# Optimization experiments

Hardware: AMD Instinct MI355X
Metric: run time of the kernel (lower is better)

Reference implementation:

```python
import jax, jax.numpy as jnp
import numpy as np

B, D, K = 8, 128, 7          # batch, num objects, per-object feature
Q = 256                      # question embedding size
G0, G1 = 511, 512            # g-layer sizes
F1, F2, OUT = 512, 1024, 16  # f-layer sizes


def setup_inputs() -> dict:
    key = jax.random.key(0)
    ks = jax.random.split(key, 14)
    def lin(kw, kb, fan_in, fan_out):
        lim = 1.0 / np.sqrt(fan_in)
        w = jax.random.uniform(kw, (fan_in, fan_out), jnp.float32, -lim, lim)
        b = jax.random.uniform(kb, (fan_out,), jnp.float32, -lim, lim)
        return w, b
    x = jax.random.normal(ks[0], (B, D, K), jnp.float32)
    qst = jax.random.normal(ks[1], (B, Q), jnp.float32)
    g0_w, g0_b = lin(ks[2], ks[3], 2 * K, G0)
    g1_w, g1_b = lin(ks[4], ks[5], G0 + Q, G1)
    f1_w, f1_b = lin(ks[6], ks[7], G1, F1)
    f2_w, f2_b = lin(ks[8], ks[9], F1, F2)
    f3_w, f3_b = lin(ks[10], ks[11], F2, OUT)
    return {"x": x, "qst": qst,
            "g0_w": g0_w, "g0_b": g0_b, "g1_w": g1_w, "g1_b": g1_b,
            "f1_w": f1_w, "f1_b": f1_b, "f2_w": f2_w, "f2_b": f2_b,
            "f3_w": f3_w, "f3_b": f3_b}


def reference(x, qst, g0_w, g0_b, g1_w, g1_b, f1_w, f1_b, f2_w, f2_b, f3_w, f3_b):
    b, d, k = x.shape
    # all-pairs: torch x_i[b,a,c,:]=x[b,c,:], x_j[b,a,c,:]=x[b,a,:]
    x_i = jnp.broadcast_to(x[:, None, :, :], (b, d, d, k))
    x_j = jnp.broadcast_to(x[:, :, None, :], (b, d, d, k))
    pairs = jnp.concatenate([x_i, x_j], axis=-1)            # (b,d,d,2k)
    h = jax.nn.relu(pairs @ g0_w + g0_b)                    # (b,d,d,G0)
    q = jnp.broadcast_to(qst[:, None, None, :], (b, d, d, qst.shape[-1]))
    h = jnp.concatenate([h, q], axis=-1)                    # (b,d,d,G0+Q)
    h = jax.nn.relu(h @ g1_w + g1_b)                        # (b,d,d,G1)
    x_g = h.sum(axis=(1, 2))                                # sum over d^2 pairs -> (b,G1)
    f = jax.nn.relu(x_g @ f1_w + f1_b)
    f = jax.nn.relu(f @ f2_w + f2_b)                        # dropout = identity (eval)
    logits = f @ f3_w + f3_b
    return jax.nn.log_softmax(logits, axis=1)
```

## Files before the change

kernel.cpp:

```cpp
#include <hip/hip_runtime.h>
#include <hip/hip_bf16.h>

#define B_  8
#define D_  128
#define K_  7
#define Q_  256
#define G0_ 511
#define G0P 512
#define G1_ 512
#define F1_ 512
#define F2_ 1024
#define OUT_ 16

typedef __bf16 bf16x8 __attribute__((ext_vector_type(8)));
typedef float  f32x4  __attribute__((ext_vector_type(4)));

#define GL2LDS(g, l) __builtin_amdgcn_global_load_lds(                        \
    (const __attribute__((address_space(1))) void*)(g),                       \
    (__attribute__((address_space(3))) void*)(l), 16, 0, 0)

__global__ void k_prep(const float* __restrict__ x, const float* __restrict__ g0w,
                       const float* __restrict__ g0b, const float* __restrict__ qst,
                       const float* __restrict__ g1w, const float* __restrict__ g1b,
                       const float* __restrict__ f1w, const float* __restrict__ f2w,
                       const float* __restrict__ f3w,
                       float* __restrict__ u, float* __restrict__ v,
                       __bf16* __restrict__ w1t, float* __restrict__ qterm,
                       float* __restrict__ xg, float* __restrict__ f1t,
                       float* __restrict__ f2t, float* __restrict__ f3t) {
    const int blk = blockIdx.x;
    const int t   = threadIdx.x;
    if (blk < 1024) {
        __shared__ float xs[8];
        if (t < K_) xs[t] = x[blk * K_ + t];
        __syncthreads();
        #pragma unroll
        for (int h = 0; h < 2; ++h) {
            const int g = t + h * 256;
            float su = 0.f, sv = 0.f;
            if (g < G0_) {
                #pragma unroll
                for (int k = 0; k < K_; ++k) {
                    su += xs[k] * g0w[k * G0_ + g];
                    sv += xs[k] * g0w[(K_ + k) * G0_ + g];
                }
                su += g0b[g];
            }
            u[blk * G0P + g] = (g < G0_) ? su : 0.f;
            v[blk * G0P + g] = (g < G0_) ? sv : 0.f;
        }
    } else if (blk < 1280) {
        __shared__ __bf16 tile[32][33];
        const int bb = blk - 1024;
        const int bx = bb & 15, by = bb >> 4;
        const int r = t >> 5, c = t & 31;
        #pragma unroll
        for (int i = 0; i < 4; ++i) {
            const int k = by * 32 + r + i * 8;
            const int n = bx * 32 + c;
            tile[r + i * 8][c] = (__bf16)((k < G0_) ? g1w[k * G1_ + n] : 0.f);
        }
        __syncthreads();
        #pragma unroll
        for (int i = 0; i < 4; ++i) {
            const int n = bx * 32 + r + i * 8;
            const int cc = (c >> 3) & 3, j = c & 7;
            const int slot = cc ^ ((n >> 1) & 3);
            w1t[by * 16384 + n * 32 + slot * 8 + j] = tile[c][r + i * 8];
        }
    } else if (blk < 1312) {
        __shared__ float qs[256];
        __shared__ float red[2][128];
        const int qb = blk - 1280;
        const int b = qb >> 2, nb = (qb & 3) << 7;
        qs[t] = qst[b * Q_ + t];
        __syncthreads();
        const int n = nb + (t & 127);
        const int qh = (t >> 7) * 128;
        float s = 0.f;
        #pragma unroll 8
        for (int q = 0; q < 128; ++q)
            s += qs[qh + q] * g1w[(G0_ + qh + q) * G1_ + n];
        red[t >> 7][t & 127] = s;
        __syncthreads();
        if (t < 128)
            qterm[b * G1_ + nb + t] = red[0][t] + red[1][t] + g1b[nb + t];
    } else if (blk < 1320) {
        const int b = blk - 1312;
        xg[b * G1_ + t] = 0.f;
        xg[b * G1_ + 256 + t] = 0.f;
    } else if (blk < 1576) {
        __shared__ float tile[32][33];
        const int j = blk - 1320;
        const int bo = j & 15, bk = j >> 4;
        const int r = t >> 5, c = t & 31;
        #pragma unroll
        for (int i = 0; i < 4; ++i)
            tile[r + i * 8][c] = f1w[(bk * 32 + r + i * 8) * F1_ + bo * 32 + c];
        __syncthreads();
        #pragma unroll
        for (int i = 0; i < 4; ++i)
            f1t[(bo * 32 + r + i * 8) * G1_ + bk * 32 + c] = tile[c][r + i * 8];
    } else if (blk < 2088) {
        __shared__ float tile[32][33];
        const int j = blk - 1576;
        const int bo = j & 31, bk = j >> 5;
        const int r = t >> 5, c = t & 31;
        #pragma unroll
        for (int i = 0; i < 4; ++i)
            tile[r + i * 8][c] = f2w[(bk * 32 + r + i * 8) * F2_ + bo * 32 + c];
        __syncthreads();
        #pragma unroll
        for (int i = 0; i < 4; ++i)
            f2t[(bo * 32 + r + i * 8) * F1_ + bk * 32 + c] = tile[c][r + i * 8];
    } else {
        const int k = (blk - 2088) * 256 + t;
        float4 r0 = *(const float4*)(f3w + k * OUT_);
        float4 r1 = *(const float4*)(f3w + k * OUT_ + 4);
        float4 r2 = *(const float4*)(f3w + k * OUT_ + 8);
        float4 r3 = *(const float4*)(f3w + k * OUT_ + 12);
        const float rr[16] = {r0.x,r0.y,r0.z,r0.w, r1.x,r1.y,r1.z,r1.w,
                              r2.x,r2.y,r2.z,r2.w, r3.x,r3.y,r3.z,r3.w};
        #pragma unroll
        for (int o = 0; o < 16; ++o) f3t[o * F2_ + k] = rr[o];
    }
}

__global__ __launch_bounds__(256, 2)
void k_pair(const float* __restrict__ u, const float* __restrict__ v,
            const __bf16* __restrict__ w1t, const float* __restrict__ qterm,
            float* __restrict__ xg) {
    __shared__ float  v_a[512];
    __shared__ __bf16 At[2][4096];
    __shared__ __bf16 Bt[2][8192];
    __shared__ float  ebuf[4][128];

    const int bid  = blockIdx.x;
    const int b    = bid >> 8;
    const int a    = (bid >> 1) & 127;
    const int nbase = (bid & 1) << 8;
    const int tid  = threadIdx.x;
    const int wave = tid >> 6, lane = tid & 63;
    const int quad = lane >> 4, l15 = lane & 15;
    const int nloc = (wave >> 1) * 128;
    const int mtg  = (wave & 1) * 4;
    const int swz  = (l15 >> 1) & 3;

    if (tid < 128)
        *(float4*)(v_a + tid * 4) = *(const float4*)(v + (b * D_ + a) * G0P + tid * 4);

    const int iw0 = wave * 4;
    const __bf16* gsrc = w1t + (size_t)(nbase + iw0 * 16 + (lane >> 2)) * 32
                             + (lane & 3) * 8;

    const int sm = tid >> 1;
    const int sk = (tid & 1) << 4;
    const float* urow = u + (b * D_ + sm) * G0P + sk;
    const int woff = (sm >> 4) * 512 + (sk >> 3) * 128 + (sm & 15) * 8;

    f32x4 acc[4][8];
    #pragma unroll
    for (int mt = 0; mt < 4; ++mt)
        #pragma unroll
        for (int nt = 0; nt < 8; ++nt)
            acc[mt][nt] = (f32x4){0.f, 0.f, 0.f, 0.f};

    float4 u0, u1, u2, u3;
    auto load_u = [&](int kq) {
        const float* p = urow + kq * 32;
        u0 = *(const float4*)p;       u1 = *(const float4*)(p + 4);
        u2 = *(const float4*)(p + 8); u3 = *(const float4*)(p + 12);
    };
    auto stage_B = [&](int buf, int kq) {
        const __bf16* g = gsrc + kq * 16384;
        __bf16* l = &Bt[buf][iw0 * 512];
        #pragma unroll
        for (int j = 0; j < 4; ++j)
            GL2LDS(g + j * 512, l + j * 512);
    };
    auto write_A = [&](int buf, int kq) {
        const float* vp = v_a + kq * 32 + sk;
        const float4 v0 = *(const float4*)vp,       v1 = *(const float4*)(vp + 4);
        const float4 v2 = *(const float4*)(vp + 8), v3 = *(const float4*)(vp + 12);
        bf16x8 h0, h1;
        h0[0] = (__bf16)fmaxf(u0.x + v0.x, 0.f);
        h0[1] = (__bf16)fmaxf(u0.y + v0.y, 0.f);
        h0[2] = (__bf16)fmaxf(u0.z + v0.z, 0.f);
        h0[3] = (__bf16)fmaxf(u0.w + v0.w, 0.f);
        h0[4] = (__bf16)fmaxf(u1.x + v1.x, 0.f);
        h0[5] = (__bf16)fmaxf(u1.y + v1.y, 0.f);
        h0[6] = (__bf16)fmaxf(u1.z + v1.z, 0.f);
        h0[7] = (__bf16)fmaxf(u1.w + v1.w, 0.f);
        h1[0] = (__bf16)fmaxf(u2.x + v2.x, 0.f);
        h1[1] = (__bf16)fmaxf(u2.y + v2.y, 0.f);
        h1[2] = (__bf16)fmaxf(u2.z + v2.z, 0.f);
        h1[3] = (__bf16)fmaxf(u2.w + v2.w, 0.f);
        h1[4] = (__bf16)fmaxf(u3.x + v3.x, 0.f);
        h1[5] = (__bf16)fmaxf(u3.y + v3.y, 0.f);
        h1[6] = (__bf16)fmaxf(u3.z + v3.z, 0.f);
        h1[7] = (__bf16)fmaxf(u3.w + v3.w, 0.f);
        __bf16* w = &At[buf][woff];
        *(bf16x8*)w = h0;
        *(bf16x8*)(w + 128) = h1;
    };

    stage_B(0, 0);
    load_u(0);
    __syncthreads();
    write_A(0, 0);
    __syncthreads();

    for (int kq = 0; kq < 16; ++kq) {
        const int buf = kq & 1;
        if (kq < 15) {
            stage_B(buf ^ 1, kq + 1);
            load_u(kq + 1);
        }
        bf16x8 af[4];
        #pragma unroll
        for (int mt = 0; mt < 4; ++mt)
            af[mt] = *(const bf16x8*)&At[buf][(mtg + mt) * 512 + lane * 8];
        bf16x8 bfr[8];
        const __bf16* btb = &Bt[buf][(nloc + l15) * 32 + ((quad ^ swz) << 3)];
        #pragma unroll
        for (int nt = 0; nt < 8; ++nt)
            bfr[nt] = *(const bf16x8*)(btb + nt * 512);
        #pragma unroll
        for (int mt = 0; mt < 4; ++mt)
            #pragma unroll
            for (int nt = 0; nt < 8; ++nt)
                acc[mt][nt] = __builtin_amdgcn_mfma_f32_16x16x32_bf16(
                    af[mt], bfr[nt], acc[mt][nt], 0, 0, 0);
        if (kq < 15) write_A(buf ^ 1, kq + 1);
        __syncthreads();
    }

    #pragma unroll
    for (int nt = 0; nt < 8; ++nt) {
        const float q = qterm[b * G1_ + nbase + nloc + nt * 16 + l15];
        float s = 0.f;
        #pragma unroll
        for (int mt = 0; mt < 4; ++mt)
            #pragma unroll
            for (int r = 0; r < 4; ++r)
                s += fmaxf(acc[mt][nt][r] + q, 0.f);
        s += __shfl_xor(s, 16, 64);
        s += __shfl_xor(s, 32, 64);
        if (quad == 0) ebuf[wave][nt * 16 + l15] = s;
    }
    __syncthreads();
    {
        const int grp = tid >> 7, nl = tid & 127;
        const float sv = ebuf[grp * 2][nl] + ebuf[grp * 2 + 1][nl];
        atomicAdd(xg + b * G1_ + nbase + grp * 128 + nl, sv);
    }
}

__global__ void k_f1(const float* __restrict__ xg, const float* __restrict__ f1t,
                     const float* __restrict__ f1b, float* __restrict__ s1g) {
    const int wave = threadIdx.x >> 6, lane = threadIdx.x & 63;
    const int id = blockIdx.x * 4 + wave;
    const int b = id >> 9, oo = id & 511;
    const float* xr = xg + b * G1_ + lane * 8;
    const float* wr = f1t + oo * G1_ + lane * 8;
    const float4 a0 = *(const float4*)xr, a1 = *(const float4*)(xr + 4);
    const float4 b0 = *(const float4*)wr, b1 = *(const float4*)(wr + 4);
    float s = a0.x*b0.x + a0.y*b0.y + a0.z*b0.z + a0.w*b0.w
            + a1.x*b1.x + a1.y*b1.y + a1.z*b1.z + a1.w*b1.w;
    #pragma unroll
    for (int off = 32; off >= 1; off >>= 1) s += __shfl_xor(s, off, 64);
    if (lane == 0) s1g[b * F1_ + oo] = fmaxf(s + f1b[oo], 0.f);
}

__global__ void k_f2(const float* __restrict__ s1g, const float* __restrict__ f2t,
                     const float* __restrict__ f2b, float* __restrict__ s2g) {
    const int wave = threadIdx.x >> 6, lane = threadIdx.x & 63;
    const int id = blockIdx.x * 4 + wave;
    const int b = id >> 10, oo = id & 1023;
    const float* xr = s1g + b * F1_ + lane * 8;
    const float* wr = f2t + oo * F1_ + lane * 8;
    const float4 a0 = *(const float4*)xr, a1 = *(const float4*)(xr + 4);
    const float4 b0 = *(const float4*)wr, b1 = *(const float4*)(wr + 4);
    float s = a0.x*b0.x + a0.y*b0.y + a0.z*b0.z + a0.w*b0.w
            + a1.x*b1.x + a1.y*b1.y + a1.z*b1.z + a1.w*b1.w;
    #pragma unroll
    for (int off = 32; off >= 1; off >>= 1) s += __shfl_xor(s, off, 64);
    if (lane == 0) s2g[b * F2_ + oo] = fmaxf(s + f2b[oo], 0.f);
}

__global__ void k_f3(const float* __restrict__ s2g, const float* __restrict__ f3t,
                     const float* __restrict__ f3b, float* __restrict__ out) {
    const int b = blockIdx.x, t = threadIdx.x;
    const int wave = t >> 6, lane = t & 63;
    __shared__ float lg[16];
    float4 xs[4];
    #pragma unroll
    for (int j = 0; j < 4; ++j)
        xs[j] = *(const float4*)(s2g + b * F2_ + lane * 16 + j * 4);
    #pragma unroll
    for (int oi = 0; oi < 4; ++oi) {
        const int o = wave * 4 + oi;
        const float* wr = f3t + o * F2_ + lane * 16;
        float s = 0.f;
        #pragma unroll
        for (int j = 0; j < 4; ++j) {
            const float4 w = *(const float4*)(wr + j * 4);
            s += xs[j].x*w.x + xs[j].y*w.y + xs[j].z*w.z + xs[j].w*w.w;
        }
        #pragma unroll
        for (int off = 32; off >= 1; off >>= 1) s += __shfl_xor(s, off, 64);
        if (lane == 0) lg[o] = s + f3b[o];
    }
    __syncthreads();
    if (t < 16) {
        float m = -1e30f;
        #pragma unroll
        for (int i = 0; i < 16; ++i) m = fmaxf(m, lg[i]);
        float se = 0.f;
        #pragma unroll
        for (int i = 0; i < 16; ++i) se += __expf(lg[i] - m);
        out[b * OUT_ + t] = lg[t] - m - logf(se);
    }
}

extern "C" void kernel_launch(void* const* d_in, const int* in_sizes, int n_in,
                              void* d_out, int out_size, void* d_ws, size_t ws_size,
                              hipStream_t stream) {
    const float* x   = (const float*)d_in[0];
    const float* qst = (const float*)d_in[1];
    const float* g0w = (const float*)d_in[2];
    const float* g0b = (const float*)d_in[3];
    const float* g1w = (const float*)d_in[4];
    const float* g1b = (const float*)d_in[5];
    const float* f1w = (const float*)d_in[6];
    const float* f1b = (const float*)d_in[7];
    const float* f2w = (const float*)d_in[8];
    const float* f2b = (const float*)d_in[9];
    const float* f3w = (const float*)d_in[10];
    const float* f3b = (const float*)d_in[11];

    char* ws = (char*)d_ws;
    float*  u     = (float*)ws;  ws += (size_t)B_ * D_ * G0P * 4;
    float*  v     = (float*)ws;  ws += (size_t)B_ * D_ * G0P * 4;
    __bf16* w1t   = (__bf16*)ws; ws += (size_t)G1_ * G0P * 2;
    float*  qterm = (float*)ws;  ws += (size_t)B_ * G1_ * 4;
    float*  xg    = (float*)ws;  ws += (size_t)B_ * G1_ * 4;
    float*  s1g   = (float*)ws;  ws += (size_t)B_ * F1_ * 4;
    float*  s2g   = (float*)ws;  ws += (size_t)B_ * F2_ * 4;
    float*  f1t   = (float*)ws;  ws += (size_t)F1_ * G1_ * 4;
    float*  f2t   = (float*)ws;  ws += (size_t)F2_ * F1_ * 4;
    float*  f3t   = (float*)ws;  ws += (size_t)OUT_ * F2_ * 4;

    k_prep<<<2092, 256, 0, stream>>>(x, g0w, g0b, qst, g1w, g1b, f1w, f2w, f3w,
                                     u, v, w1t, qterm, xg, f1t, f2t, f3t);
    k_pair<<<B_ * D_ * 2, 256, 0, stream>>>(u, v, w1t, qterm, xg);
    k_f1  <<<1024, 256, 0, stream>>>(xg, f1t, f1b, s1g);
    k_f2  <<<2048, 256, 0, stream>>>(s1g, f2t, f2b, s2g);
    k_f3  <<<B_, 256, 0, stream>>>(s2g, f3t, f3b, (float*)d_out);
}
```

Before: 193.9 us.

## Triple-buffer B tiles and use manual waitcnt barriers for deeper prefetch

Expands the B (weight) LDS staging from double to triple buffering so global-to-LDS loads are issued two k-steps ahead, and replaces __syncthreads with hand-written s_waitcnt lgkmcnt/vmcnt plus s_barrier so barriers wait only on LDS traffic rather than draining all outstanding global loads. The v-row load is also hoisted into a register and overlapped with the initial staging. This raises LDS usage by another 16KB per block, which could hurt occupancy with 2 blocks/CU, and the hand-tuned vmcnt counts risk correctness if they mismatch the issued loads.

Result: no change. 192.2 us (-0.9%).

```diff
diff --git a/kernel.cpp b/kernel.cpp
--- a/kernel.cpp
+++ b/kernel.cpp
@@ -132,7 +132,7 @@
             float* __restrict__ xg) {
     __shared__ float  v_a[512];
     __shared__ __bf16 At[2][4096];
-    __shared__ __bf16 Bt[2][8192];
+    __shared__ __bf16 Bt[3][8192];
     __shared__ float  ebuf[4][128];
 
     const int bid  = blockIdx.x;
@@ -145,9 +145,6 @@
     const int nloc = (wave >> 1) * 128;
     const int mtg  = (wave & 1) * 4;
     const int swz  = (l15 >> 1) & 3;
-
-    if (tid < 128)
-        *(float4*)(v_a + tid * 4) = *(const float4*)(v + (b * D_ + a) * G0P + tid * 4);
 
     const int iw0 = wave * 4;
     const __bf16* gsrc = w1t + (size_t)(nbase + iw0 * 16 + (lane >> 2)) * 32
@@ -204,24 +201,29 @@
         *(bf16x8*)(w + 128) = h1;
     };
 
+    float4 vq;
+    if (tid < 128) vq = *(const float4*)(v + (b * D_ + a) * G0P + tid * 4);
+    load_u(0);
+    asm volatile("" ::: "memory");
     stage_B(0, 0);
-    load_u(0);
-    __syncthreads();
+    stage_B(1, 1);
+    if (tid < 128) *(float4*)(v_a + tid * 4) = vq;
+    asm volatile("s_waitcnt lgkmcnt(0)\n\ts_barrier" ::: "memory");
     write_A(0, 0);
-    __syncthreads();
-
+    asm volatile("s_waitcnt vmcnt(4) lgkmcnt(0)\n\ts_barrier" ::: "memory");
+
+    int bcur = 0, bnxt = 1, bstg = 2;
     for (int kq = 0; kq < 16; ++kq) {
-        const int buf = kq & 1;
-        if (kq < 15) {
-            stage_B(buf ^ 1, kq + 1);
-            load_u(kq + 1);
-        }
+        const int abuf = kq & 1;
+        if (kq < 15) load_u(kq + 1);
+        asm volatile("" ::: "memory");
+        if (kq < 14) stage_B(bstg, kq + 2);
         bf16x8 af[4];
         #pragma unroll
         for (int mt = 0; mt < 4; ++mt)
-            af[mt] = *(const bf16x8*)&At[buf][(mtg + mt) * 512 + lane * 8];
+            af[mt] = *(const bf16x8*)&At[abuf][(mtg + mt) * 512 + lane * 8];
         bf16x8 bfr[8];
-        const __bf16* btb = &Bt[buf][(nloc + l15) * 32 + ((quad ^ swz) << 3)];
+        const __bf16* btb = &Bt[bcur][(nloc + l15) * 32 + ((quad ^ swz) << 3)];
         #pragma unroll
         for (int nt = 0; nt < 8; ++nt)
             bfr[nt] = *(const bf16x8*)(btb + nt * 512);
@@ -231,8 +233,9 @@
             for (int nt = 0; nt < 8; ++nt)
                 acc[mt][nt] = __builtin_amdgcn_mfma_f32_16x16x32_bf16(
                     af[mt], bfr[nt], acc[mt][nt], 0, 0, 0);
-        if (kq < 15) write_A(buf ^ 1, kq + 1);
-        __syncthreads();
+        if (kq < 15) write_A(abuf ^ 1, kq + 1);
+        asm volatile("s_waitcnt lgkmcnt(0)\n\ts_barrier" ::: "memory");
+        const int t3 = bcur; bcur = bnxt; bnxt = bstg; bstg = t3;
     }
 
     #pragma unroll
```
